# Performance work log

Hardware: AMD Instinct MI355X
Metric: run time of the kernel (lower is better)

The kernel has to match this reference:

```python
import jax, jax.numpy as jnp
import numpy as np

B, L, HID, NH, E = 2, 2048, 1024, 16, 128
HS = HID // NH  # attention_head_size = 64 (scores scaled by sqrt(HS), NOT sqrt(E))


def setup_inputs() -> dict:
    key = jax.random.key(0)
    ks = jax.random.split(key, 8)
    s = 0.02
    return {
        "hidden_states": jax.random.normal(ks[0], (B, L, HID), jnp.float32),
        "attention_mask": jnp.zeros((B, 1, 1, L), jnp.float32),
        "rel_pos": jax.random.normal(ks[1], (1, NH, L, L), jnp.float32),
        "Wq": jax.random.normal(ks[2], (NH * E, HID), jnp.float32) * s,
        "bq": jnp.zeros((NH * E,), jnp.float32),
        "Wk": jax.random.normal(ks[3], (NH * E, HID), jnp.float32) * s,
        "Wv": jax.random.normal(ks[4], (HID, HID), jnp.float32) * s,
        "bv": jnp.zeros((HID,), jnp.float32),
        "Wg": jax.random.normal(ks[5], (8, E), jnp.float32) * s,
        "bg": jnp.zeros((8,), jnp.float32),
        "eco_a": jnp.ones((1, NH, 1, 1), jnp.float32),
    }


def reference(hidden_states, attention_mask, rel_pos, Wq, bq, Wk, Wv, bv, Wg, bg, eco_a):
    b, l, _ = hidden_states.shape
    # projections -> [B, H, L, E] / [B, H, L, HS]
    q = (hidden_states @ Wq.T + bq).reshape(b, l, NH, E).transpose(0, 2, 1, 3)
    k = (hidden_states @ Wk.T).reshape(b, l, NH, E).transpose(0, 2, 1, 3)
    v = (hidden_states @ Wv.T + bv).reshape(b, l, NH, HS).transpose(0, 2, 1, 3)
    scores = jnp.einsum('bhqe,bhke->bhqk', q, k) / jnp.asarray(np.sqrt(HS), q.dtype)
    scores = scores + attention_mask
    # gated relative-position bias: gate_ur_linear(q) -> [B,H,L,2,4] -> sum -> sigmoid
    g = jax.nn.sigmoid((q @ Wg.T + bg).reshape(b, NH, l, 2, 4).sum(-1))
    gate_u, gate_r = g[..., 0:1], g[..., 1:2]  # each [B,H,L,1]
    gate_u_1 = gate_u * (gate_r * eco_a - 1.0) + 2.0
    scores = scores + gate_u_1 * rel_pos
    probs = jax.nn.softmax(scores, axis=-1)  # dropout p=0 -> identity
    ctx = jnp.einsum('bhqk,bhkd->bhqd', probs, v)
    return ctx.transpose(0, 2, 1, 3).reshape(b, l, HID)
```

## Files before the change

kernel.cpp:

```cpp
#include <hip/hip_runtime.h>
#include <hip/hip_bf16.h>
#include <stdint.h>

#define Bn 2
#define Ln 2048
#define HIDn 1024
#define NHn 16
#define En 128
#define HSn 64

typedef unsigned short u16;
typedef short s16x8 __attribute__((ext_vector_type(8)));
typedef float f32x4 __attribute__((ext_vector_type(4)));

__device__ __forceinline__ u16 f2bf(float f) {
  union { float f; uint32_t u; } v; v.f = f;
  uint32_t r = (v.u + 0x7fffu + ((v.u >> 16) & 1u)) >> 16;
  return (u16)r;
}
__device__ __forceinline__ float bf2f(u16 b) {
  union { uint32_t u; float f; } v; v.u = ((uint32_t)b) << 16;
  return v.f;
}
__device__ __forceinline__ void async16(const void* g, void* l) {
  __builtin_amdgcn_global_load_lds((const __attribute__((address_space(1))) void*)g,
                                   (__attribute__((address_space(3))) void*)l, 16, 0, 0);
}

__global__ void castbf(const float* __restrict__ in, u16* __restrict__ out, int n) {
  int i = (blockIdx.x * blockDim.x + threadIdx.x) * 4;
  if (i >= n) return;
  float4 v = *(const float4*)(in + i);
  u16 o[4] = {f2bf(v.x), f2bf(v.y), f2bf(v.z), f2bf(v.w)};
  *(uint64_t*)(out + i) = *(uint64_t*)o;
}

__global__ void wgprep(const float* __restrict__ Wg, float* __restrict__ wgu,
                       float* __restrict__ wgr) {
  int e = threadIdx.x;
  wgu[e] = Wg[0 * 128 + e] + Wg[1 * 128 + e] + Wg[2 * 128 + e] + Wg[3 * 128 + e];
  wgr[e] = Wg[4 * 128 + e] + Wg[5 * 128 + e] + Wg[6 * 128 + e] + Wg[7 * 128 + e];
}

__global__ __launch_bounds__(256) void qkv_gemm(
    const u16* __restrict__ A, const u16* __restrict__ W,
    const float* __restrict__ bq, const float* __restrict__ bv,
    u16* __restrict__ qb, u16* __restrict__ kb, u16* __restrict__ vt) {
  __shared__ union {
    struct { u16 a[128 * 32]; u16 b[128 * 32]; } st;
    u16 cq[64][140];
    u16 cv[128][72];
  } lds;
  const int tid = threadIdx.x, lane = tid & 63, w = tid >> 6;
  const int quad = lane >> 4, ln = lane & 15;
  const int bx = blockIdx.x, by = blockIdx.y;
  const int m0 = (w >> 1) * 64, n0 = (w & 1) * 64;
  f32x4 acc[4][4];
  for (int i = 0; i < 4; ++i)
    for (int j = 0; j < 4; ++j) acc[i][j] = (f32x4)0.0f;

  for (int k0 = 0; k0 < 1024; k0 += 32) {
    __syncthreads();
    for (int cc = 0; cc < 2; ++cc) {
      int c = w * 2 + cc;
      int row = c * 16 + (lane >> 2);
      int ke = (lane & 3) * 8;
      async16(A + (size_t)(by * 128 + row) * 1024 + k0 + ke, lds.st.a + c * 512);
      async16(W + (size_t)(bx * 128 + row) * 1024 + k0 + ke, lds.st.b + c * 512);
    }
    __syncthreads();
    s16x8 a[4], bf[4];
    for (int i = 0; i < 4; ++i)
      a[i] = *(const s16x8*)&lds.st.a[(m0 + i * 16 + ln) * 32 + quad * 8];
    for (int j = 0; j < 4; ++j)
      bf[j] = *(const s16x8*)&lds.st.b[(n0 + j * 16 + ln) * 32 + quad * 8];
    for (int i = 0; i < 4; ++i)
      for (int j = 0; j < 4; ++j)
        acc[i][j] = __builtin_amdgcn_mfma_f32_16x16x32_bf16(a[i], bf[j], acc[i][j], 0, 0, 0);
  }

  float bias[4];
#pragma unroll
  for (int j = 0; j < 4; ++j) {
    int col = bx * 128 + n0 + j * 16 + ln;
    bias[j] = (bx < 16) ? bq[col] : (bx >= 32 ? bv[col - 4096] : 0.0f);
  }

  if (bx < 32) {
    for (int half = 0; half < 2; ++half) {
      __syncthreads();
      if ((w >> 1) == half) {
#pragma unroll
        for (int i = 0; i < 4; ++i)
#pragma unroll
          for (int j = 0; j < 4; ++j)
#pragma unroll
            for (int r = 0; r < 4; ++r)
              lds.cq[i * 16 + quad * 4 + r][n0 + j * 16 + ln] = f2bf(acc[i][j][r] + bias[j]);
      }
      __syncthreads();
#pragma unroll
      for (int it = 0; it < 4; ++it) {
        int slot = it * 256 + tid;
        int row = slot >> 4, seg = slot & 15;
        int rowg = by * 128 + half * 64 + row;
        int b = rowg >> 11, l = rowg & 2047;
        uint4 d = *(const uint4*)&lds.cq[row][seg * 8];
        if (bx < 16) {
          *(uint4*)(qb + ((size_t)(b * 16 + bx) * 2048 + l) * 128 + seg * 8) = d;
        } else {
          int sg = (seg ^ (l & 15)) & 15;
          *(uint4*)(kb + ((size_t)(b * 16 + (bx - 16)) * 2048 + l) * 128 + sg * 8) = d;
        }
      }
    }
  } else {
    for (int half = 0; half < 2; ++half) {
      __syncthreads();
      if ((w >> 1) == half) {
#pragma unroll
        for (int i = 0; i < 4; ++i)
#pragma unroll
          for (int j = 0; j < 4; ++j)
#pragma unroll
            for (int r = 0; r < 4; ++r)
              lds.cv[n0 + j * 16 + ln][i * 16 + quad * 4 + r] = f2bf(acc[i][j][r] + bias[j]);
      }
      __syncthreads();
      int rowg = by * 128 + half * 64;
      int b = rowg >> 11, lbase = rowg & 2047;
#pragma unroll
      for (int it = 0; it < 4; ++it) {
        int slot = it * 256 + tid;
        int row = slot >> 3, seg = slot & 7;
        int c2 = (bx - 32) * 128 + row;
        int h = c2 >> 6, hs = c2 & 63;
        int sg = seg ^ (hs & 7);
        uint4 d = *(const uint4*)&lds.cv[row][seg * 8];
        *(uint4*)(vt + ((size_t)(b * 16 + h) * 64 + hs) * 2048 + lbase + sg * 8) = d;
      }
    }
  }
}

__global__ void gate_kernel(const u16* __restrict__ qb, const float* __restrict__ wgu,
                            const float* __restrict__ wgr, const float* __restrict__ bg,
                            const float* __restrict__ eco, float* __restrict__ gate) {
  int t = blockIdx.x * 256 + threadIdx.x;
  int h = (t >> 11) & 15;
  const u16* q = qb + (size_t)t * 128;
  float u = bg[0] + bg[1] + bg[2] + bg[3];
  float rr = bg[4] + bg[5] + bg[6] + bg[7];
  for (int e = 0; e < 128; e += 8) {
    uint4 d = *(const uint4*)(q + e);
    const u16* p = (const u16*)&d;
#pragma unroll
    for (int jj = 0; jj < 8; ++jj) {
      float f = bf2f(p[jj]);
      u += f * wgu[e + jj];
      rr += f * wgr[e + jj];
    }
  }
  float gu = 1.0f / (1.0f + __expf(-u));
  float gr = 1.0f / (1.0f + __expf(-rr));
  gate[t] = gu * (gr * eco[h] - 1.0f) + 2.0f;
}

__global__ __launch_bounds__(256, 4) void attn_kernel(
    const u16* __restrict__ qb, const u16* __restrict__ kb, const u16* __restrict__ vt,
    const float* __restrict__ mask, const float* __restrict__ relpos,
    const float* __restrict__ gate, float* __restrict__ out) {
  __shared__ u16 sK[64 * 128];
  __shared__ u16 sVt[64 * 64];
  __shared__ u16 sP[4][16 * 72];

  const int tid = threadIdx.x, lane = tid & 63, w = tid >> 6;
  const int quad = lane >> 4, ln = lane & 15;
  const int bx = blockIdx.x, h = blockIdx.y;
  const int qt = bx >> 1, b = bx & 1;
  const int q0 = qt * 64;
  const u16* qptr = qb + (size_t)(b * NHn + h) * Ln * En;
  const u16* kptr = kb + (size_t)(b * NHn + h) * Ln * En;
  const u16* vptr = vt + (size_t)(b * NHn + h) * HSn * Ln;
  const float* rp = relpos + (size_t)h * Ln * Ln + (size_t)q0 * Ln;
  const float* mk = mask + (size_t)b * Ln;
  const float* gt = gate + (size_t)(b * NHn + h) * Ln;

  s16x8 aq[4];
  {
    const u16* qrow = qptr + (size_t)(q0 + w * 16 + ln) * En;
#pragma unroll
    for (int es = 0; es < 4; ++es)
      aq[es] = *(const s16x8*)(qrow + (es * 4 + quad) * 8);
  }
  float gv[4];
#pragma unroll
  for (int r = 0; r < 4; ++r) gv[r] = gt[q0 + w * 16 + quad * 4 + r];

  float l_part[4] = {0.0f, 0.0f, 0.0f, 0.0f};
  f32x4 O[4];
#pragma unroll
  for (int j = 0; j < 4; ++j) O[j] = (f32x4)0.0f;

  for (int kt = 0; kt < Ln / 64; ++kt) {
    const int kbase = kt * 64;
    __syncthreads();
#pragma unroll
    for (int cc = 0; cc < 4; ++cc) {
      int c = w * 4 + cc;
      async16(kptr + (size_t)(kbase + c * 4 + (lane >> 4)) * En + (lane & 15) * 8,
              sK + c * 512);
    }
#pragma unroll
    for (int cc = 0; cc < 2; ++cc) {
      int c = w * 2 + cc;
      async16(vptr + (size_t)(c * 8 + (lane >> 3)) * Ln + kbase + (lane & 7) * 8,
              sVt + c * 512);
    }
    float rpv[4][4];
    {
      const float* rpr = rp + (size_t)(w * 16 + quad * 4) * Ln + kbase + ln;
#pragma unroll
      for (int r = 0; r < 4; ++r)
#pragma unroll
        for (int j = 0; j < 4; ++j) rpv[j][r] = rpr[(size_t)r * Ln + j * 16];
    }
    float mv[4];
#pragma unroll
    for (int j = 0; j < 4; ++j) mv[j] = mk[kbase + j * 16 + ln];
    __syncthreads();

    f32x4 S[4];
#pragma unroll
    for (int j = 0; j < 4; ++j) S[j] = (f32x4)0.0f;
#pragma unroll
    for (int es = 0; es < 4; ++es) {
#pragma unroll
      for (int j = 0; j < 4; ++j) {
        s16x8 bk = *(const s16x8*)&sK[(j * 16 + ln) * 128 + (((es * 4 + quad) ^ ln) & 15) * 8];
        S[j] = __builtin_amdgcn_mfma_f32_16x16x32_bf16(aq[es], bk, S[j], 0, 0, 0);
      }
    }
#pragma unroll
    for (int j = 0; j < 4; ++j) {
#pragma unroll
      for (int r = 0; r < 4; ++r) {
        float p = __expf(S[j][r] * 0.125f + mv[j] + gv[r] * rpv[j][r]);
        l_part[r] += p;
        sP[w][(quad * 4 + r) * 72 + j * 16 + ln] = f2bf(p);
      }
    }
#pragma unroll
    for (int ks = 0; ks < 2; ++ks) {
      s16x8 ap = *(const s16x8*)&sP[w][ln * 72 + ks * 32 + quad * 8];
#pragma unroll
      for (int j = 0; j < 4; ++j) {
        s16x8 bv_ = *(const s16x8*)&sVt[(j * 16 + ln) * 64 + (((ks * 4 + quad) ^ (ln & 7)) & 7) * 8];
        O[j] = __builtin_amdgcn_mfma_f32_16x16x32_bf16(ap, bv_, O[j], 0, 0, 0);
      }
    }
  }

#pragma unroll
  for (int r = 0; r < 4; ++r) {
    float l = l_part[r];
    l += __shfl_xor(l, 1, 64);
    l += __shfl_xor(l, 2, 64);
    l += __shfl_xor(l, 4, 64);
    l += __shfl_xor(l, 8, 64);
    float inv = 1.0f / l;
    int qrow = q0 + w * 16 + quad * 4 + r;
    float* op = out + ((size_t)b * Ln + qrow) * HIDn + h * 64;
#pragma unroll
    for (int j = 0; j < 4; ++j) op[j * 16 + ln] = O[j][r] * inv;
  }
}

extern "C" void kernel_launch(void* const* d_in, const int* in_sizes, int n_in,
                              void* d_out, int out_size, void* d_ws, size_t ws_size,
                              hipStream_t stream) {
  const float* hs = (const float*)d_in[0];
  const float* mask = (const float*)d_in[1];
  const float* relpos = (const float*)d_in[2];
  const float* Wq = (const float*)d_in[3];
  const float* bq = (const float*)d_in[4];
  const float* Wk = (const float*)d_in[5];
  const float* Wv = (const float*)d_in[6];
  const float* bv = (const float*)d_in[7];
  const float* Wg = (const float*)d_in[8];
  const float* bg = (const float*)d_in[9];
  const float* eco = (const float*)d_in[10];
  float* out = (float*)d_out;

  char* ws = (char*)d_ws;
  u16* hsb = (u16*)ws;
  u16* wb = (u16*)(ws + (8ull << 20));
  u16* qb = (u16*)(ws + (18ull << 20));
  u16* kb = (u16*)(ws + (34ull << 20));
  u16* vt = (u16*)(ws + (50ull << 20));
  float* gate = (float*)(ws + (58ull << 20));
  float* wgu = (float*)(ws + (58ull << 20) + (1ull << 19));
  float* wgr = wgu + 128;

  castbf<<<4096, 256, 0, stream>>>(hs, hsb, 4096 * 1024);
  castbf<<<2048, 256, 0, stream>>>(Wq, wb, 2048 * 1024);
  castbf<<<2048, 256, 0, stream>>>(Wk, wb + 2048 * 1024, 2048 * 1024);
  castbf<<<1024, 256, 0, stream>>>(Wv, wb + 4096 * 1024, 1024 * 1024);
  wgprep<<<1, 128, 0, stream>>>(Wg, wgu, wgr);
  qkv_gemm<<<dim3(40, 32), 256, 0, stream>>>(hsb, wb, bq, bv, qb, kb, vt);
  gate_kernel<<<256, 256, 0, stream>>>(qb, wgu, wgr, bg, eco, gate);
  attn_kernel<<<dim3(64, 16), 256, 0, stream>>>(qb, kb, vt, mask, relpos, gate, out);
}
```

Before: 546.9 us.

## Double-buffer K/V tiles, prefetch rel_pos, and use 128-row query tiles

```diff
diff --git a/kernel.cpp b/kernel.cpp
--- a/kernel.cpp
+++ b/kernel.cpp
@@ -166,19 +166,19 @@
   gate[t] = gu * (gr * eco[h] - 1.0f) + 2.0f;
 }
 
-__global__ __launch_bounds__(256, 4) void attn_kernel(
+__global__ __launch_bounds__(512, 4) void attn_kernel(
     const u16* __restrict__ qb, const u16* __restrict__ kb, const u16* __restrict__ vt,
     const float* __restrict__ mask, const float* __restrict__ relpos,
     const float* __restrict__ gate, float* __restrict__ out) {
-  __shared__ u16 sK[64 * 128];
-  __shared__ u16 sVt[64 * 64];
-  __shared__ u16 sP[4][16 * 72];
+  __shared__ u16 sK[2][64 * 128];
+  __shared__ u16 sVt[2][64 * 64];
+  __shared__ u16 sP[8][16 * 72];
 
   const int tid = threadIdx.x, lane = tid & 63, w = tid >> 6;
   const int quad = lane >> 4, ln = lane & 15;
   const int bx = blockIdx.x, h = blockIdx.y;
   const int qt = bx >> 1, b = bx & 1;
-  const int q0 = qt * 64;
+  const int q0 = qt * 128;
   const u16* qptr = qb + (size_t)(b * NHn + h) * Ln * En;
   const u16* kptr = kb + (size_t)(b * NHn + h) * Ln * En;
   const u16* vptr = vt + (size_t)(b * NHn + h) * HSn * Ln;
@@ -202,33 +202,38 @@
 #pragma unroll
   for (int j = 0; j < 4; ++j) O[j] = (f32x4)0.0f;
 
-  for (int kt = 0; kt < Ln / 64; ++kt) {
+  auto stage = [&](int buf, int kt) {
     const int kbase = kt * 64;
-    __syncthreads();
-#pragma unroll
-    for (int cc = 0; cc < 4; ++cc) {
-      int c = w * 4 + cc;
-      async16(kptr + (size_t)(kbase + c * 4 + (lane >> 4)) * En + (lane & 15) * 8,
-              sK + c * 512);
-    }
 #pragma unroll
     for (int cc = 0; cc < 2; ++cc) {
       int c = w * 2 + cc;
-      async16(vptr + (size_t)(c * 8 + (lane >> 3)) * Ln + kbase + (lane & 7) * 8,
-              sVt + c * 512);
-    }
-    float rpv[4][4];
-    {
-      const float* rpr = rp + (size_t)(w * 16 + quad * 4) * Ln + kbase + ln;
-#pragma unroll
-      for (int r = 0; r < 4; ++r)
-#pragma unroll
-        for (int j = 0; j < 4; ++j) rpv[j][r] = rpr[(size_t)r * Ln + j * 16];
-    }
+      async16(kptr + (size_t)(kbase + c * 4 + (lane >> 4)) * En + (lane & 15) * 8,
+              &sK[buf][c * 512]);
+    }
+    async16(vptr + (size_t)(w * 8 + (lane >> 3)) * Ln + kbase + (lane & 7) * 8,
+            &sVt[buf][w * 512]);
+  };
+  auto ldrp = [&](int kt, float (&rv)[4][4]) {
+    const float* rpr = rp + (size_t)(w * 16 + quad * 4) * Ln + kt * 64 + ln;
+#pragma unroll
+    for (int r = 0; r < 4; ++r)
+#pragma unroll
+      for (int j = 0; j < 4; ++j) rv[j][r] = rpr[(size_t)r * Ln + j * 16];
+  };
+
+  stage(0, 0);
+  float rpc[4][4];
+  ldrp(0, rpc);
+
+  for (int kt = 0; kt < Ln / 64; ++kt) {
+    const int cur = kt & 1;
+    __syncthreads();
+    if (kt + 1 < Ln / 64) stage(cur ^ 1, kt + 1);
     float mv[4];
 #pragma unroll
-    for (int j = 0; j < 4; ++j) mv[j] = mk[kbase + j * 16 + ln];
-    __syncthreads();
+    for (int j = 0; j < 4; ++j) mv[j] = mk[kt * 64 + j * 16 + ln];
+    float rpn[4][4];
+    if (kt + 1 < Ln / 64) ldrp(kt + 1, rpn);
 
     f32x4 S[4];
 #pragma unroll
@@ -237,7 +242,7 @@
     for (int es = 0; es < 4; ++es) {
 #pragma unroll
       for (int j = 0; j < 4; ++j) {
-        s16x8 bk = *(const s16x8*)&sK[(j * 16 + ln) * 128 + (((es * 4 + quad) ^ ln) & 15) * 8];
+        s16x8 bk = *(const s16x8*)&sK[cur][(j * 16 + ln) * 128 + (((es * 4 + quad) ^ ln) & 15) * 8];
         S[j] = __builtin_amdgcn_mfma_f32_16x16x32_bf16(aq[es], bk, S[j], 0, 0, 0);
       }
     }
@@ -245,7 +250,7 @@
     for (int j = 0; j < 4; ++j) {
 #pragma unroll
       for (int r = 0; r < 4; ++r) {
-        float p = __expf(S[j][r] * 0.125f + mv[j] + gv[r] * rpv[j][r]);
+        float p = __expf(S[j][r] * 0.125f + mv[j] + gv[r] * rpc[j][r]);
         l_part[r] += p;
         sP[w][(quad * 4 + r) * 72 + j * 16 + ln] = f2bf(p);
       }
@@ -255,9 +260,15 @@
       s16x8 ap = *(const s16x8*)&sP[w][ln * 72 + ks * 32 + quad * 8];
 #pragma unroll
       for (int j = 0; j < 4; ++j) {
-        s16x8 bv_ = *(const s16x8*)&sVt[(j * 16 + ln) * 64 + (((ks * 4 + quad) ^ (ln & 7)) & 7) * 8];
+        s16x8 bv_ = *(const s16x8*)&sVt[cur][(j * 16 + ln) * 64 + (((ks * 4 + quad) ^ (ln & 7)) & 7) * 8];
         O[j] = __builtin_amdgcn_mfma_f32_16x16x32_bf16(ap, bv_, O[j], 0, 0, 0);
       }
+    }
+    if (kt + 1 < Ln / 64) {
+#pragma unroll
+      for (int j = 0; j < 4; ++j)
+#pragma unroll
+        for (int r = 0; r < 4; ++r) rpc[j][r] = rpn[j][r];
     }
   }
 
@@ -309,5 +320,5 @@
   wgprep<<<1, 128, 0, stream>>>(Wg, wgu, wgr);
   qkv_gemm<<<dim3(40, 32), 256, 0, stream>>>(hsb, wb, bq, bv, qb, kb, vt);
   gate_kernel<<<256, 256, 0, stream>>>(qb, wgu, wgr, bg, eco, gate);
-  attn_kernel<<<dim3(64, 16), 256, 0, stream>>>(qb, kb, vt, mask, relpos, gate, out);
-}
+  attn_kernel<<<dim3(32, 16), 512, 0, stream>>>(qb, kb, vt, mask, relpos, gate, out);
+}
```

After: 553.9 us. Within noise of the previous version (+1.3%).

## Rework attention kernel with 32x32 MFMA, double-buffered K/V, staged rel_pos

Applied to the files above, without the earlier changes.

```diff
diff --git a/kernel.cpp b/kernel.cpp
--- a/kernel.cpp
+++ b/kernel.cpp
@@ -12,6 +12,7 @@
 typedef unsigned short u16;
 typedef short s16x8 __attribute__((ext_vector_type(8)));
 typedef float f32x4 __attribute__((ext_vector_type(4)));
+typedef float f32x16 __attribute__((ext_vector_type(16)));
 
 __device__ __forceinline__ u16 f2bf(float f) {
   union { float f; uint32_t u; } v; v.f = f;
@@ -166,113 +167,163 @@
   gate[t] = gu * (gr * eco[h] - 1.0f) + 2.0f;
 }
 
-__global__ __launch_bounds__(256, 4) void attn_kernel(
-    const u16* __restrict__ qb, const u16* __restrict__ kb, const u16* __restrict__ vt,
+__global__ __launch_bounds__(256, 2) void attn_kernel(
+    const u16* __restrict__ qb, const u16* __restrict__ kbp, const u16* __restrict__ vt,
     const float* __restrict__ mask, const float* __restrict__ relpos,
     const float* __restrict__ gate, float* __restrict__ out) {
-  __shared__ u16 sK[64 * 128];
-  __shared__ u16 sVt[64 * 64];
-  __shared__ u16 sP[4][16 * 72];
+  __shared__ u16 sK[2][64 * 128];
+  __shared__ u16 sVt[2][64 * 64];
+  __shared__ float sRP[128 * 64];
 
   const int tid = threadIdx.x, lane = tid & 63, w = tid >> 6;
-  const int quad = lane >> 4, ln = lane & 15;
+  const int q5 = lane & 31, hi = lane >> 5;
   const int bx = blockIdx.x, h = blockIdx.y;
   const int qt = bx >> 1, b = bx & 1;
-  const int q0 = qt * 64;
+  const int q0 = qt * 128;
   const u16* qptr = qb + (size_t)(b * NHn + h) * Ln * En;
-  const u16* kptr = kb + (size_t)(b * NHn + h) * Ln * En;
+  const u16* kptr = kbp + (size_t)(b * NHn + h) * Ln * En;
   const u16* vptr = vt + (size_t)(b * NHn + h) * HSn * Ln;
-  const float* rp = relpos + (size_t)h * Ln * Ln + (size_t)q0 * Ln;
+  const float* rpb = relpos + (size_t)h * Ln * Ln + (size_t)q0 * Ln;
   const float* mk = mask + (size_t)b * Ln;
   const float* gt = gate + (size_t)(b * NHn + h) * Ln;
 
-  s16x8 aq[4];
+  s16x8 aq[8];
   {
-    const u16* qrow = qptr + (size_t)(q0 + w * 16 + ln) * En;
-#pragma unroll
-    for (int es = 0; es < 4; ++es)
-      aq[es] = *(const s16x8*)(qrow + (es * 4 + quad) * 8);
-  }
-  float gv[4];
-#pragma unroll
-  for (int r = 0; r < 4; ++r) gv[r] = gt[q0 + w * 16 + quad * 4 + r];
-
-  float l_part[4] = {0.0f, 0.0f, 0.0f, 0.0f};
-  f32x4 O[4];
-#pragma unroll
-  for (int j = 0; j < 4; ++j) O[j] = (f32x4)0.0f;
-
-  for (int kt = 0; kt < Ln / 64; ++kt) {
+    const u16* qrow = qptr + (size_t)(q0 + w * 32 + q5) * En;
+#pragma unroll
+    for (int es = 0; es < 8; ++es)
+      aq[es] = *(const s16x8*)(qrow + es * 16 + hi * 8);
+  }
+  const float gv = gt[q0 + w * 32 + q5];
+
+  float l_part = 0.0f;
+  f32x16 O0 = (f32x16)0.0f, O1 = (f32x16)0.0f;
+
+  auto stage = [&](int buf, int kt) {
     const int kbase = kt * 64;
-    __syncthreads();
 #pragma unroll
     for (int cc = 0; cc < 4; ++cc) {
       int c = w * 4 + cc;
       async16(kptr + (size_t)(kbase + c * 4 + (lane >> 4)) * En + (lane & 15) * 8,
-              sK + c * 512);
+              &sK[buf][c * 512]);
     }
 #pragma unroll
     for (int cc = 0; cc < 2; ++cc) {
       int c = w * 2 + cc;
       async16(vptr + (size_t)(c * 8 + (lane >> 3)) * Ln + kbase + (lane & 7) * 8,
-              sVt + c * 512);
-    }
-    float rpv[4][4];
-    {
-      const float* rpr = rp + (size_t)(w * 16 + quad * 4) * Ln + kbase + ln;
-#pragma unroll
-      for (int r = 0; r < 4; ++r)
-#pragma unroll
-        for (int j = 0; j < 4; ++j) rpv[j][r] = rpr[(size_t)r * Ln + j * 16];
-    }
-    float mv[4];
-#pragma unroll
-    for (int j = 0; j < 4; ++j) mv[j] = mk[kbase + j * 16 + ln];
+              &sVt[buf][c * 512]);
+    }
+  };
+  auto rpload = [&](int kt, float4 (&rg)[8]) {
+#pragma unroll
+    for (int i = 0; i < 8; ++i) {
+      int s = i * 256 + tid;
+      int qq = s >> 4, gc = s & 15;
+      rg[i] = *(const float4*)(rpb + (size_t)qq * Ln + kt * 64 + gc * 4);
+    }
+  };
+  auto rpwrite = [&](const float4 (&rg)[8]) {
+#pragma unroll
+    for (int i = 0; i < 8; ++i) {
+      int s = i * 256 + tid;
+      int qq = s >> 4, gc = s & 15;
+      *(float4*)&sRP[qq * 64 + ((gc ^ (qq & 15)) * 4)] = rg[i];
+    }
+  };
+
+  const int NT = Ln / 64;
+  stage(0, 0);
+  float4 rg[8];
+  rpload(0, rg);
+  rpwrite(rg);
+
+  for (int kt = 0; kt < NT; ++kt) {
+    const int cur = kt & 1;
     __syncthreads();
-
-    f32x4 S[4];
-#pragma unroll
-    for (int j = 0; j < 4; ++j) S[j] = (f32x4)0.0f;
-#pragma unroll
-    for (int es = 0; es < 4; ++es) {
-#pragma unroll
-      for (int j = 0; j < 4; ++j) {
-        s16x8 bk = *(const s16x8*)&sK[(j * 16 + ln) * 128 + (((es * 4 + quad) ^ ln) & 15) * 8];
-        S[j] = __builtin_amdgcn_mfma_f32_16x16x32_bf16(aq[es], bk, S[j], 0, 0, 0);
-      }
-    }
-#pragma unroll
-    for (int j = 0; j < 4; ++j) {
-#pragma unroll
-      for (int r = 0; r < 4; ++r) {
-        float p = __expf(S[j][r] * 0.125f + mv[j] + gv[r] * rpv[j][r]);
-        l_part[r] += p;
-        sP[w][(quad * 4 + r) * 72 + j * 16 + ln] = f2bf(p);
-      }
-    }
-#pragma unroll
-    for (int ks = 0; ks < 2; ++ks) {
-      s16x8 ap = *(const s16x8*)&sP[w][ln * 72 + ks * 32 + quad * 8];
-#pragma unroll
-      for (int j = 0; j < 4; ++j) {
-        s16x8 bv_ = *(const s16x8*)&sVt[(j * 16 + ln) * 64 + (((ks * 4 + quad) ^ (ln & 7)) & 7) * 8];
-        O[j] = __builtin_amdgcn_mfma_f32_16x16x32_bf16(ap, bv_, O[j], 0, 0, 0);
-      }
-    }
-  }
-
-#pragma unroll
-  for (int r = 0; r < 4; ++r) {
-    float l = l_part[r];
-    l += __shfl_xor(l, 1, 64);
-    l += __shfl_xor(l, 2, 64);
-    l += __shfl_xor(l, 4, 64);
-    l += __shfl_xor(l, 8, 64);
-    float inv = 1.0f / l;
-    int qrow = q0 + w * 16 + quad * 4 + r;
-    float* op = out + ((size_t)b * Ln + qrow) * HIDn + h * 64;
-#pragma unroll
-    for (int j = 0; j < 4; ++j) op[j * 16 + ln] = O[j][r] * inv;
+    if (kt + 1 < NT) {
+      stage(cur ^ 1, kt + 1);
+      rpload(kt + 1, rg);
+    }
+
+    const u16* sKc = sK[cur];
+    f32x16 S0 = (f32x16)0.0f, S1 = (f32x16)0.0f;
+    __builtin_amdgcn_s_setprio(1);
+#pragma unroll
+    for (int es = 0; es < 8; ++es) {
+      int gsw = ((es * 2 + hi) ^ (q5 & 15)) * 8;
+      s16x8 ak0 = *(const s16x8*)&sKc[q5 * 128 + gsw];
+      S0 = __builtin_amdgcn_mfma_f32_32x32x16_bf16(ak0, aq[es], S0, 0, 0, 0);
+      s16x8 ak1 = *(const s16x8*)&sKc[(32 + q5) * 128 + gsw];
+      S1 = __builtin_amdgcn_mfma_f32_32x32x16_bf16(ak1, aq[es], S1, 0, 0, 0);
+    }
+    __builtin_amdgcn_s_setprio(0);
+
+    uint32_t pkv[16];
+#pragma unroll
+    for (int kbi = 0; kbi < 2; ++kbi) {
+      const f32x16 Sa = kbi ? S1 : S0;
+#pragma unroll
+      for (int g = 0; g < 4; ++g) {
+        f32x4 rp4 = *(const f32x4*)&sRP[(w * 32 + q5) * 64 +
+                                        (((kbi * 8 + g * 2 + hi) ^ (q5 & 15)) * 4)];
+        float4 mv4 = *(const float4*)(mk + kt * 64 + kbi * 32 + g * 8 + hi * 4);
+        float p0 = __expf(fmaf(gv, rp4[0], fmaf(Sa[4 * g + 0], 0.125f, mv4.x)));
+        float p1 = __expf(fmaf(gv, rp4[1], fmaf(Sa[4 * g + 1], 0.125f, mv4.y)));
+        float p2 = __expf(fmaf(gv, rp4[2], fmaf(Sa[4 * g + 2], 0.125f, mv4.z)));
+        float p3 = __expf(fmaf(gv, rp4[3], fmaf(Sa[4 * g + 3], 0.125f, mv4.w)));
+        l_part += (p0 + p1) + (p2 + p3);
+        uint32_t c0, c1;
+        asm("v_cvt_pk_bf16_f32 %0, %1, %2" : "=v"(c0) : "v"(p0), "v"(p1));
+        asm("v_cvt_pk_bf16_f32 %0, %1, %2" : "=v"(c1) : "v"(p2), "v"(p3));
+        pkv[kbi * 8 + g * 2] = c0;
+        pkv[kbi * 8 + g * 2 + 1] = c1;
+      }
+    }
+#pragma unroll
+    for (int base = 0; base < 16; base += 8) {
+      asm volatile("v_permlane32_swap_b32 %0, %1" : "+v"(pkv[base + 0]), "+v"(pkv[base + 2]));
+      asm volatile("v_permlane32_swap_b32 %0, %1" : "+v"(pkv[base + 1]), "+v"(pkv[base + 3]));
+      asm volatile("v_permlane32_swap_b32 %0, %1" : "+v"(pkv[base + 4]), "+v"(pkv[base + 6]));
+      asm volatile("v_permlane32_swap_b32 %0, %1" : "+v"(pkv[base + 5]), "+v"(pkv[base + 7]));
+    }
+
+    if (kt + 1 < NT) {
+#pragma unroll
+      for (int i = 0; i < 8; ++i)
+        asm volatile("" : "+v"(rg[i].x), "+v"(rg[i].y), "+v"(rg[i].z), "+v"(rg[i].w));
+    }
+    __syncthreads();
+    if (kt + 1 < NT) rpwrite(rg);
+
+    const u16* sVc = sVt[cur];
+    __builtin_amdgcn_s_setprio(1);
+#pragma unroll
+    for (int ks2 = 0; ks2 < 4; ++ks2) {
+      union { uint32_t u[4]; s16x8 v; } pu;
+      pu.u[0] = pkv[ks2 * 4 + 0];
+      pu.u[1] = pkv[ks2 * 4 + 1];
+      pu.u[2] = pkv[ks2 * 4 + 2];
+      pu.u[3] = pkv[ks2 * 4 + 3];
+      s16x8 pa = pu.v;
+      int gsw = ((ks2 * 2 + hi) ^ (q5 & 7)) * 8;
+      s16x8 bv0 = *(const s16x8*)&sVc[q5 * 64 + gsw];
+      O0 = __builtin_amdgcn_mfma_f32_32x32x16_bf16(pa, bv0, O0, 0, 0, 0);
+      s16x8 bv1 = *(const s16x8*)&sVc[(32 + q5) * 64 + gsw];
+      O1 = __builtin_amdgcn_mfma_f32_32x32x16_bf16(pa, bv1, O1, 0, 0, 0);
+    }
+    __builtin_amdgcn_s_setprio(0);
+  }
+
+  float lt = l_part + __shfl_xor(l_part, 32, 64);
+  float inv = 1.0f / lt;
+#pragma unroll
+  for (int i = 0; i < 16; ++i) {
+    int qr = (i & 3) + 8 * (i >> 2) + 4 * hi;
+    float iv = __shfl(inv, qr, 64);
+    int qg = q0 + w * 32 + qr;
+    float* orow = out + ((size_t)b * Ln + qg) * HIDn + h * 64;
+    orow[q5] = O0[i] * iv;
+    orow[32 + q5] = O1[i] * iv;
   }
 }
 
@@ -309,5 +360,5 @@
   wgprep<<<1, 128, 0, stream>>>(Wg, wgu, wgr);
   qkv_gemm<<<dim3(40, 32), 256, 0, stream>>>(hsb, wb, bq, bv, qb, kb, vt);
   gate_kernel<<<256, 256, 0, stream>>>(qb, wgu, wgr, bg, eco, gate);
-  attn_kernel<<<dim3(64, 16), 256, 0, stream>>>(qb, kb, vt, mask, relpos, gate, out);
-}
+  attn_kernel<<<dim3(32, 16), 256, 0, stream>>>(qb, kb, vt, mask, relpos, gate, out);
+}
```

Result: no change. 551.0 us (+0.8%).
